# Kernel tuning notes

Hardware: AMD Instinct MI355X
Metric: run time of the kernel (lower is better)

The kernel has to match this reference:

```python
import jax, jax.numpy as jnp
import numpy as np

N = 100_000
E = 1_600_000
F_IN = 128
HID = 64
HEADS = 2
HC = HID // HEADS  # 32 per-head channels
EPS = 1e-5
NEG_SLOPE = 0.2


def _layer_norm(x, g, b):
    mu = jnp.mean(x, axis=-1, keepdims=True)
    var = jnp.mean(jnp.square(x - mu), axis=-1, keepdims=True)
    return (x - mu) * jax.lax.rsqrt(var + EPS) * g + b


def _batch_norm(x, g, b):
    # training-mode batch statistics over the node axis (biased variance)
    mu = jnp.mean(x, axis=0, keepdims=True)
    var = jnp.mean(jnp.square(x - mu), axis=0, keepdims=True)
    return (x - mu) * jax.lax.rsqrt(var + EPS) * g + b


def _gcn_conv(x, src, dst, W, bias, n):
    # PyG GCNConv: self-loops already included in (src, dst); symmetric norm
    deg = jax.ops.segment_sum(jnp.ones_like(src, dtype=x.dtype), dst, num_segments=n)
    dinv = jnp.where(deg > 0, jax.lax.rsqrt(deg), 0.0)
    norm = dinv[src] * dinv[dst]                      # [E2]
    xw = x @ W                                        # [N, out]
    msg = xw[src] * norm[:, None]                     # gather + scale
    out = jax.ops.segment_sum(msg, dst, num_segments=n)
    return out + bias


def _gat_conv(x, src, dst, W, att_src, att_dst, bias, n):
    # PyG GATConv, heads=HEADS, concat=True (self-loops included in src/dst)
    xw = (x @ W).reshape(n, HEADS, HC)                # [N, H, C]
    a_s = jnp.sum(xw * att_src, axis=-1)              # [N, H]
    a_d = jnp.sum(xw * att_dst, axis=-1)              # [N, H]
    e = jax.nn.leaky_relu(a_s[src] + a_d[dst], NEG_SLOPE)  # [E2, H]
    m = jax.ops.segment_max(e, dst, num_segments=n)   # per-target max for stability
    e = jnp.exp(e - m[dst])
    denom = jax.ops.segment_sum(e, dst, num_segments=n)
    alpha = e / (denom[dst] + 1e-16)                  # neighborhood softmax
    out = jax.ops.segment_sum(xw[src] * alpha[:, :, None], dst, num_segments=n)
    return out.reshape(n, HEADS * HC) + bias


def setup_inputs() -> dict:
    key = jax.random.key(0)
    ks = jax.random.split(key, 20)
    f32 = jnp.float32
    d = {}
    d["accessibility_features"] = jax.random.normal(ks[0], (N, F_IN), dtype=f32)
    d["edge_index"] = jax.random.randint(ks[1], (2, E), 0, N, dtype=jnp.int64)
    # LayerNorm
    d["ln_g"] = jnp.ones((F_IN,), f32); d["ln_b"] = jnp.zeros((F_IN,), f32)
    # feature encoder
    d["enc_w1"] = jax.random.normal(ks[2], (F_IN, HID), f32) * (2.0 / (F_IN + HID)) ** 0.5
    d["enc_b1"] = jnp.zeros((HID,), f32)
    d["enc_w2"] = jax.random.normal(ks[3], (HID, HID), f32) * (1.0 / HID) ** 0.5
    d["enc_b2"] = jnp.zeros((HID,), f32)
    # GCN 1
    d["gcn1_w"] = jax.random.normal(ks[4], (HID, HID), f32) * (1.0 / HID) ** 0.5
    d["gcn1_b"] = jnp.zeros((HID,), f32)
    d["bn1_g"] = jnp.ones((HID,), f32); d["bn1_b"] = jnp.zeros((HID,), f32)
    # GAT
    d["gat_w"] = jax.random.normal(ks[5], (HID, HEADS * HC), f32) * (1.0 / HID) ** 0.5
    d["gat_as"] = jax.random.normal(ks[6], (HEADS, HC), f32) * 0.1
    d["gat_ad"] = jax.random.normal(ks[7], (HEADS, HC), f32) * 0.1
    d["gat_b"] = jnp.zeros((HEADS * HC,), f32)
    d["bn2_g"] = jnp.ones((HID,), f32); d["bn2_b"] = jnp.zeros((HID,), f32)
    # GCN 2 -> hidden//2
    d["gcn2_w"] = jax.random.normal(ks[8], (HID, HID // 2), f32) * (2.0 / (HID + HID // 2)) ** 0.5
    d["gcn2_b"] = jnp.zeros((HID // 2,), f32)
    d["bn3_g"] = jnp.ones((HID // 2,), f32); d["bn3_b"] = jnp.zeros((HID // 2,), f32)
    # prediction head
    d["pred_w1"] = jax.random.normal(ks[9], (HID // 2, HID // 4), f32) * (2.0 / (HID // 2 + HID // 4)) ** 0.5
    d["pred_b1"] = jnp.zeros((HID // 4,), f32)
    d["pred_w2"] = jax.random.normal(ks[10], (HID // 4, 1), f32) * (2.0 / (HID // 4 + 1)) ** 0.5
    d["pred_b2"] = jnp.zeros((1,), f32)
    return d


def reference(accessibility_features, edge_index, ln_g, ln_b, enc_w1, enc_b1,
              enc_w2, enc_b2, gcn1_w, gcn1_b, bn1_g, bn1_b, gat_w, gat_as,
              gat_ad, gat_b, bn2_g, bn2_b, gcn2_w, gcn2_b, bn3_g, bn3_b,
              pred_w1, pred_b1, pred_w2, pred_b2):
    n = accessibility_features.shape[0]
    loops = jnp.arange(n, dtype=edge_index.dtype)
    src = jnp.concatenate([edge_index[0], loops])   # add self-loops once
    dst = jnp.concatenate([edge_index[1], loops])

    x = _layer_norm(accessibility_features, ln_g, ln_b)
    x = jax.nn.relu(x @ enc_w1 + enc_b1)            # dropout = identity (eval)
    x = jax.nn.relu(x @ enc_w2 + enc_b2)

    x = _gcn_conv(x, src, dst, gcn1_w, gcn1_b, n)
    x = jax.nn.relu(_batch_norm(x, bn1_g, bn1_b))

    xa = _gat_conv(x, src, dst, gat_w, gat_as, gat_ad, gat_b, n)
    xa = jax.nn.relu(_batch_norm(xa, bn2_g, bn2_b))

    x = _gcn_conv(xa, src, dst, gcn2_w, gcn2_b, n)
    x = jax.nn.relu(_batch_norm(x, bn3_g, bn3_b))

    h = jax.nn.relu(x @ pred_w1 + pred_b1)
    svi = jax.nn.sigmoid((h @ pred_w2 + pred_b2).squeeze(-1))
    return svi
```

## Files before the change

kernel.cpp:

```cpp
#include <hip/hip_runtime.h>
#include <math.h>

#define F_IN 128
#define HID  64
#define EPS  1e-5f
#define NSLOPE 0.2f
#define BSH 9
#define MAXBUK 1024
#define EPB 4096
#define SPB 4096

__device__ __forceinline__ float lrelu(float x) { return x > 0.f ? x : NSLOPE * x; }


__global__ __launch_bounds__(256) void k_buk_count(const int* __restrict__ ei,
                                                   int* __restrict__ bukcnt, int E, int nbuk) {
  __shared__ int lc[MAXBUK];
  for (int k = threadIdx.x; k < nbuk; k += 256) lc[k] = 0;
  __syncthreads();
  int base = blockIdx.x * EPB, end = min(E, base + EPB);
  for (int t = base + threadIdx.x; t < end; t += 256) atomicAdd(&lc[ei[E + t] >> BSH], 1);
  __syncthreads();
  for (int k = threadIdx.x; k < nbuk; k += 256)
    if (lc[k]) atomicAdd(&bukcnt[k], lc[k]);
}

__global__ void k_buk_scan(const int* __restrict__ bukcnt, int* __restrict__ bukbase, int nbuk) {
  __shared__ int l[MAXBUK + 1];
  for (int k = threadIdx.x; k < nbuk; k += blockDim.x) l[k] = bukcnt[k];
  __syncthreads();
  if (threadIdx.x == 0) {
    int r = 0;
    for (int k = 0; k < nbuk; ++k) { int t = l[k]; l[k] = r; r += t; }
    l[nbuk] = r;
  }
  __syncthreads();
  for (int k = threadIdx.x; k <= nbuk; k += blockDim.x) bukbase[k] = l[k];
}

__global__ __launch_bounds__(256) void k_buk_scatter(const int* __restrict__ ei,
                                                     const int* __restrict__ bukbase,
                                                     int* __restrict__ bukcur,
                                                     int2* __restrict__ pairs, int E, int nbuk) {
  __shared__ int lc[MAXBUK];
  __shared__ int lbase[MAXBUK];
  for (int k = threadIdx.x; k < nbuk; k += 256) lc[k] = 0;
  __syncthreads();
  int base = blockIdx.x * EPB, end = min(E, base + EPB);
  for (int t = base + threadIdx.x; t < end; t += 256) atomicAdd(&lc[ei[E + t] >> BSH], 1);
  __syncthreads();
  for (int k = threadIdx.x; k < nbuk; k += 256) {
    int c = lc[k];
    lbase[k] = c ? atomicAdd(&bukcur[k], c) : 0;
  }
  __syncthreads();
  for (int k = threadIdx.x; k < nbuk; k += 256) lc[k] = 0;
  __syncthreads();
  for (int t = base + threadIdx.x; t < end; t += 256) {
    int s = ei[t], d = ei[E + t];
    int b = d >> BSH;
    int o = atomicAdd(&lc[b], 1);
    pairs[bukbase[b] + lbase[b] + o] = make_int2(s, d);
  }
}

__global__ __launch_bounds__(256) void k_buk_deg(const int2* __restrict__ pairs,
                                                 const int* __restrict__ bukbase,
                                                 int* __restrict__ ideg, int N) {
  __shared__ int ldeg[1 << BSH];
  int b = blockIdx.x;
  for (int k = threadIdx.x; k < (1 << BSH); k += 256) ldeg[k] = 0;
  __syncthreads();
  int s0 = bukbase[b], s1 = bukbase[b + 1], nb = b << BSH;
  for (int t = s0 + threadIdx.x; t < s1; t += 256) atomicAdd(&ldeg[pairs[t].y - nb], 1);
  __syncthreads();
  for (int k = threadIdx.x; k < (1 << BSH); k += 256) {
    int node = nb + k;
    if (node < N) ideg[node] = ldeg[k];
  }
}

__global__ __launch_bounds__(256) void k_scan_sums(const int* __restrict__ ideg,
                                                   int* __restrict__ bsum, int N) {
  __shared__ int red[256];
  int base = blockIdx.x * SPB + threadIdx.x * 16;
  int s = 0;
#pragma unroll
  for (int j = 0; j < 16; ++j) { int i = base + j; if (i < N) s += ideg[i] + 1; }
  red[threadIdx.x] = s;
  __syncthreads();
  for (int o = 128; o; o >>= 1) {
    if (threadIdx.x < o) red[threadIdx.x] += red[threadIdx.x + o];
    __syncthreads();
  }
  if (threadIdx.x == 0) bsum[blockIdx.x] = red[0];
}

__global__ void k_scan_tops(int* __restrict__ bsum, int nb) {
  __shared__ int l[MAXBUK];
  for (int k = threadIdx.x; k < nb; k += blockDim.x) l[k] = bsum[k];
  __syncthreads();
  if (threadIdx.x == 0) {
    int r = 0;
    for (int k = 0; k < nb; ++k) { int t = l[k]; l[k] = r; r += t; }
  }
  __syncthreads();
  for (int k = threadIdx.x; k < nb; k += blockDim.x) bsum[k] = l[k];
}

__global__ __launch_bounds__(256) void k_scan_apply(const int* __restrict__ ideg,
                                                    const int* __restrict__ bsum,
                                                    int* __restrict__ rowstart,
                                                    float* __restrict__ dinv,
                                                    int* __restrict__ csr, int N) {
  __shared__ int pre[256];
  int base = blockIdx.x * SPB + threadIdx.x * 16;
  int deg[16];
  int s = 0;
#pragma unroll
  for (int j = 0; j < 16; ++j) {
    int i = base + j;
    int d = (i < N) ? ideg[i] + 1 : 0;
    deg[j] = d; s += d;
  }
  pre[threadIdx.x] = s;
  __syncthreads();
  for (int o = 1; o < 256; o <<= 1) {
    int v = (threadIdx.x >= o) ? pre[threadIdx.x - o] : 0;
    __syncthreads();
    pre[threadIdx.x] += v;
    __syncthreads();
  }
  int off = bsum[blockIdx.x] + pre[threadIdx.x] - s;
#pragma unroll
  for (int j = 0; j < 16; ++j) {
    int i = base + j;
    if (i < N) {
      rowstart[i] = off;
      dinv[i] = rsqrtf((float)deg[j]);
      csr[off] = i;
      off += deg[j];
    }
  }
}

__global__ __launch_bounds__(256) void k_buk_fill(const int2* __restrict__ pairs,
                                                  const int* __restrict__ bukbase,
                                                  const int* __restrict__ rowstart,
                                                  int* __restrict__ csr) {
  __shared__ int lcur[1 << BSH];
  int b = blockIdx.x;
  for (int k = threadIdx.x; k < (1 << BSH); k += 256) lcur[k] = 0;
  __syncthreads();
  int s0 = bukbase[b], s1 = bukbase[b + 1], nb = b << BSH;
  for (int t = s0 + threadIdx.x; t < s1; t += 256) {
    int2 pr = pairs[t];
    int o = atomicAdd(&lcur[pr.y - nb], 1);
    csr[rowstart[pr.y] + 1 + o] = pr.x;
  }
}

__global__ void k_precomp(const float* __restrict__ w1, const float* __restrict__ ln_g,
                          const float* __restrict__ ln_b, const float* __restrict__ b1,
                          float* __restrict__ w1g, float* __restrict__ c1,
                          float* __restrict__ cb) {
  int j = threadIdx.x;
  float c1v = 0.f, cbv = 0.f;
  for (int k = 0; k < F_IN; ++k) {
    float w = w1[k * HID + j];
    float wg = ln_g[k] * w;
    w1g[k * HID + j] = wg;
    c1v += wg;
    cbv += ln_b[k] * w;
  }
  c1[j] = c1v;
  cb[j] = cbv + b1[j];
}

__global__ __launch_bounds__(256) void k_enc(
    const float* __restrict__ x, const float* __restrict__ w1g,
    const float* __restrict__ c1, const float* __restrict__ cb,
    const float* __restrict__ w2, const float* __restrict__ b2,
    float* __restrict__ out, int N) {
  __shared__ float shl[256 * 65];
  int i = blockIdx.x * 256 + threadIdx.x;
  if (i >= N) return;
  const float4* xr = (const float4*)(x + (size_t)i * F_IN);
  float acc[HID];
#pragma unroll
  for (int j = 0; j < HID; ++j) acc[j] = 0.f;
  float s = 0.f, q = 0.f;
#pragma unroll 1
  for (int c = 0; c < F_IN / 4; ++c) {
    float4 xv = xr[c];
    s += xv.x + xv.y + xv.z + xv.w;
    q += xv.x * xv.x + xv.y * xv.y + xv.z * xv.z + xv.w * xv.w;
    const float* wr = w1g + c * 4 * HID;
#pragma unroll
    for (int e = 0; e < 4; ++e) {
      float xe = (e == 0) ? xv.x : (e == 1) ? xv.y : (e == 2) ? xv.z : xv.w;
      const float4* w4 = (const float4*)(wr + e * HID);
#pragma unroll
      for (int j4 = 0; j4 < HID / 4; ++j4) {
        float4 wv = w4[j4];
        acc[j4 * 4 + 0] += xe * wv.x;
        acc[j4 * 4 + 1] += xe * wv.y;
        acc[j4 * 4 + 2] += xe * wv.z;
        acc[j4 * 4 + 3] += xe * wv.w;
      }
    }
  }
  float mu = s * (1.f / F_IN);
  float var = q * (1.f / F_IN) - mu * mu;
  float rs = rsqrtf(var + EPS);
  int base = threadIdx.x * 65;
#pragma unroll
  for (int j = 0; j < HID; ++j)
    shl[base + j] = fmaxf(rs * (acc[j] - mu * c1[j]) + cb[j], 0.f);
  float acc2[HID];
#pragma unroll
  for (int j = 0; j < HID; ++j) acc2[j] = b2[j];
#pragma unroll 4
  for (int j = 0; j < HID; ++j) {
    float hj = shl[base + j];
    const float4* w4 = (const float4*)(w2 + j * HID);
#pragma unroll
    for (int c4 = 0; c4 < HID / 4; ++c4) {
      float4 wv = w4[c4];
      acc2[c4 * 4 + 0] += hj * wv.x;
      acc2[c4 * 4 + 1] += hj * wv.y;
      acc2[c4 * 4 + 2] += hj * wv.z;
      acc2[c4 * 4 + 3] += hj * wv.w;
    }
  }
  float4* o4 = (float4*)(out + (size_t)i * HID);
#pragma unroll
  for (int c4 = 0; c4 < HID / 4; ++c4)
    o4[c4] = make_float4(fmaxf(acc2[c4 * 4 + 0], 0.f), fmaxf(acc2[c4 * 4 + 1], 0.f),
                         fmaxf(acc2[c4 * 4 + 2], 0.f), fmaxf(acc2[c4 * 4 + 3], 0.f));
}

template <int FOUT, bool GAT, bool BNIN>
__global__ __launch_bounds__(256) void k_gemm_reg(
    const float* __restrict__ x, const float* __restrict__ w,
    const float* __restrict__ stats,
    const float* __restrict__ atts, const float* __restrict__ atd,
    float* __restrict__ out, float* __restrict__ a_s, float* __restrict__ a_d, int N) {
  int i = blockIdx.x * 256 + threadIdx.x;
  if (i >= N) return;
  const float4* xr = (const float4*)(x + (size_t)i * HID);
  float acc[FOUT];
#pragma unroll
  for (int j = 0; j < FOUT; ++j) acc[j] = 0.f;
#pragma unroll 1
  for (int c = 0; c < HID / 4; ++c) {
    float4 xv = xr[c];
    if (BNIN) {
      xv.x = fmaxf(xv.x * stats[c * 4 + 0] + stats[HID + c * 4 + 0], 0.f);
      xv.y = fmaxf(xv.y * stats[c * 4 + 1] + stats[HID + c * 4 + 1], 0.f);
      xv.z = fmaxf(xv.z * stats[c * 4 + 2] + stats[HID + c * 4 + 2], 0.f);
      xv.w = fmaxf(xv.w * stats[c * 4 + 3] + stats[HID + c * 4 + 3], 0.f);
    }
    const float* wr = w + c * 4 * FOUT;
#pragma unroll
    for (int e = 0; e < 4; ++e) {
      float xe = (e == 0) ? xv.x : (e == 1) ? xv.y : (e == 2) ? xv.z : xv.w;
      const float4* w4 = (const float4*)(wr + e * FOUT);
#pragma unroll
      for (int j4 = 0; j4 < FOUT / 4; ++j4) {
        float4 wv = w4[j4];
        acc[j4 * 4 + 0] += xe * wv.x;
        acc[j4 * 4 + 1] += xe * wv.y;
        acc[j4 * 4 + 2] += xe * wv.z;
        acc[j4 * 4 + 3] += xe * wv.w;
      }
    }
  }
  float4* o4 = (float4*)(out + (size_t)i * FOUT);
#pragma unroll
  for (int c4 = 0; c4 < FOUT / 4; ++c4)
    o4[c4] = make_float4(acc[c4 * 4 + 0], acc[c4 * 4 + 1], acc[c4 * 4 + 2], acc[c4 * 4 + 3]);
  if (GAT) {
    float s0 = 0.f, s1 = 0.f, d0 = 0.f, d1 = 0.f;
#pragma unroll
    for (int c = 0; c < 32; ++c) { s0 += acc[c] * atts[c]; d0 += acc[c] * atd[c]; }
#pragma unroll
    for (int c = 32; c < 64; ++c) { s1 += acc[c] * atts[c]; d1 += acc[c] * atd[c]; }
    a_s[i * 2] = s0; a_s[i * 2 + 1] = s1;
    a_d[i * 2] = d0; a_d[i * 2 + 1] = d1;
  }
}

__global__ __launch_bounds__(256) void k_gcn_pull64(
    const int* __restrict__ csr, const int* __restrict__ rowstart, const int* __restrict__ ideg,
    const float* __restrict__ dinv, const float* __restrict__ xw,
    float* __restrict__ out, int N) {
  int wave = threadIdx.x >> 6, lane = threadIdx.x & 63;
  int i = blockIdx.x * 4 + wave;
  if (i >= N) return;
  int row = rowstart[i], dg = ideg[i] + 1;
  float did = dinv[i];
  float acc = 0.f;
  for (int base = 0; base < dg; base += 64) {
    int cnt = min(64, dg - base);
    int sid = (lane < cnt) ? csr[row + base + lane] : 0;
    int n = 0;
    for (; n + 4 <= cnt; n += 4) {
      int s0 = __shfl(sid, n), s1 = __shfl(sid, n + 1);
      int s2 = __shfl(sid, n + 2), s3 = __shfl(sid, n + 3);
      acc += dinv[s0] * did * xw[s0 * 64 + lane] + dinv[s1] * did * xw[s1 * 64 + lane] +
             dinv[s2] * did * xw[s2 * 64 + lane] + dinv[s3] * did * xw[s3 * 64 + lane];
    }
    for (; n < cnt; ++n) {
      int s0 = __shfl(sid, n);
      acc += dinv[s0] * did * xw[s0 * 64 + lane];
    }
  }
  out[i * 64 + lane] = acc;
}

__global__ __launch_bounds__(256) void k_gcn_pull32(
    const int* __restrict__ csr, const int* __restrict__ rowstart, const int* __restrict__ ideg,
    const float* __restrict__ dinv, const float* __restrict__ xw,
    float* __restrict__ out, int N) {
  int wave = threadIdx.x >> 6, lane = threadIdx.x & 63;
  int half = lane >> 5, lf = lane & 31;
  int i = (blockIdx.x * 4 + wave) * 2 + half;
  if (i >= N) return;
  int row = rowstart[i], dg = ideg[i] + 1;
  float did = dinv[i];
  float acc = 0.f;
  for (int base = 0; base < dg; base += 32) {
    int cnt = min(32, dg - base);
    int sid = (lf < cnt) ? csr[row + base + lf] : 0;
    int n = 0;
    for (; n + 2 <= cnt; n += 2) {
      int s0 = __shfl(sid, n, 32), s1 = __shfl(sid, n + 1, 32);
      acc += dinv[s0] * did * xw[s0 * 32 + lf] + dinv[s1] * did * xw[s1 * 32 + lf];
    }
    for (; n < cnt; ++n) {
      int s0 = __shfl(sid, n, 32);
      acc += dinv[s0] * did * xw[s0 * 32 + lf];
    }
  }
  out[i * 32 + lf] = acc;
}

__global__ __launch_bounds__(256) void k_gat_attn(
    const int* __restrict__ csr, const int* __restrict__ rowstart, const int* __restrict__ ideg,
    const float* __restrict__ a_s, const float* __restrict__ a_d,
    float* __restrict__ m_, float* __restrict__ rden, int N) {
  int wave = threadIdx.x >> 6, lane = threadIdx.x & 63;
  int i = blockIdx.x * 4 + wave;
  if (i >= N) return;
  int row = rowstart[i], dg = ideg[i] + 1;
  float ad0 = a_d[i * 2], ad1 = a_d[i * 2 + 1];
  if (dg <= 64) {
    float e0 = -1e30f, e1 = -1e30f;
    if (lane < dg) {
      int s = csr[row + lane];
      e0 = lrelu(a_s[s * 2] + ad0);
      e1 = lrelu(a_s[s * 2 + 1] + ad1);
    }
    float m0 = e0, m1 = e1;
#pragma unroll
    for (int o = 32; o; o >>= 1) { m0 = fmaxf(m0, __shfl_xor(m0, o)); m1 = fmaxf(m1, __shfl_xor(m1, o)); }
    float s0 = (lane < dg) ? __expf(e0 - m0) : 0.f;
    float s1 = (lane < dg) ? __expf(e1 - m1) : 0.f;
#pragma unroll
    for (int o = 32; o; o >>= 1) { s0 += __shfl_xor(s0, o); s1 += __shfl_xor(s1, o); }
    if (lane == 0) {
      m_[i * 2] = m0; m_[i * 2 + 1] = m1;
      rden[i * 2] = 1.f / (s0 + 1e-16f); rden[i * 2 + 1] = 1.f / (s1 + 1e-16f);
    }
  } else {
    float m0 = -1e30f, m1 = -1e30f;
    for (int base = 0; base < dg; base += 64)
      if (base + lane < dg) {
        int s = csr[row + base + lane];
        m0 = fmaxf(m0, lrelu(a_s[s * 2] + ad0));
        m1 = fmaxf(m1, lrelu(a_s[s * 2 + 1] + ad1));
      }
#pragma unroll
    for (int o = 32; o; o >>= 1) { m0 = fmaxf(m0, __shfl_xor(m0, o)); m1 = fmaxf(m1, __shfl_xor(m1, o)); }
    float s0 = 0.f, s1 = 0.f;
    for (int base = 0; base < dg; base += 64)
      if (base + lane < dg) {
        int s = csr[row + base + lane];
        s0 += __expf(lrelu(a_s[s * 2] + ad0) - m0);
        s1 += __expf(lrelu(a_s[s * 2 + 1] + ad1) - m1);
      }
#pragma unroll
    for (int o = 32; o; o >>= 1) { s0 += __shfl_xor(s0, o); s1 += __shfl_xor(s1, o); }
    if (lane == 0) {
      m_[i * 2] = m0; m_[i * 2 + 1] = m1;
      rden[i * 2] = 1.f / (s0 + 1e-16f); rden[i * 2 + 1] = 1.f / (s1 + 1e-16f);
    }
  }
}

__global__ __launch_bounds__(256) void k_gat_pv(
    const int* __restrict__ csr, const int* __restrict__ rowstart, const int* __restrict__ ideg,
    const float* __restrict__ a_s, const float* __restrict__ a_d,
    const float* __restrict__ m_, const float* __restrict__ rden,
    const float* __restrict__ xw, float* __restrict__ out, int N) {
  int wave = threadIdx.x >> 6, lane = threadIdx.x & 63;
  int i = blockIdx.x * 4 + wave;
  if (i >= N) return;
  int row = rowstart[i], dg = ideg[i] + 1;
  int h = lane >> 5;
  float adh = a_d[i * 2 + h], mh = m_[i * 2 + h], rh = rden[i * 2 + h];
  float acc = 0.f;
  for (int base = 0; base < dg; base += 64) {
    int cnt = min(64, dg - base);
    int sid = (lane < cnt) ? csr[row + base + lane] : 0;
    int n = 0;
    for (; n + 2 <= cnt; n += 2) {
      int s0 = __shfl(sid, n), s1 = __shfl(sid, n + 1);
      float al0 = __expf(lrelu(a_s[s0 * 2 + h] + adh) - mh) * rh;
      float al1 = __expf(lrelu(a_s[s1 * 2 + h] + adh) - mh) * rh;
      acc += al0 * xw[s0 * HID + lane] + al1 * xw[s1 * HID + lane];
    }
    for (; n < cnt; ++n) {
      int s0 = __shfl(sid, n);
      float al0 = __expf(lrelu(a_s[s0 * 2 + h] + adh) - mh) * rh;
      acc += al0 * xw[s0 * HID + lane];
    }
  }
  out[i * HID + lane] = acc;
}

template <int F>
__global__ __launch_bounds__(256) void k_bn_reduce(const float* __restrict__ x,
                                                   float* __restrict__ partials, int N) {
  __shared__ float sS[F], sQ[F];
  int tid = threadIdx.x;
  int t = blockIdx.x * 256 + tid;
  int stride = gridDim.x * 256;
  int total4 = N * F / 4;
  int f0 = (t * 4) % F;
  float s0 = 0, s1 = 0, s2 = 0, s3 = 0, q0 = 0, q1 = 0, q2 = 0, q3 = 0;
  for (int c = t; c < total4; c += stride) {
    float4 v = ((const float4*)x)[c];
    s0 += v.x; q0 += v.x * v.x;
    s1 += v.y; q1 += v.y * v.y;
    s2 += v.z; q2 += v.z * v.z;
    s3 += v.w; q3 += v.w * v.w;
  }
  if (tid < F) { sS[tid] = 0.f; sQ[tid] = 0.f; }
  __syncthreads();
  atomicAdd(&sS[f0], s0);     atomicAdd(&sQ[f0], q0);
  atomicAdd(&sS[f0 + 1], s1); atomicAdd(&sQ[f0 + 1], q1);
  atomicAdd(&sS[f0 + 2], s2); atomicAdd(&sQ[f0 + 2], q2);
  atomicAdd(&sS[f0 + 3], s3); atomicAdd(&sQ[f0 + 3], q3);
  __syncthreads();
  if (tid < F) {
    partials[blockIdx.x * 2 * F + tid]     = sS[tid];
    partials[blockIdx.x * 2 * F + F + tid] = sQ[tid];
  }
}

template <int F>
__global__ void k_bn_finalize(const float* __restrict__ partials, int nblk,
                              float* __restrict__ stats, const float* __restrict__ g,
                              const float* __restrict__ b, int N) {
  int f = threadIdx.x;
  if (f >= F) return;
  float s = 0.f, q = 0.f;
  for (int k = 0; k < nblk; ++k) {
    s += partials[k * 2 * F + f];
    q += partials[k * 2 * F + F + f];
  }
  float mu = s / (float)N;
  float var = q / (float)N - mu * mu;
  float sc = rsqrtf(var + EPS) * g[f];
  stats[f] = sc;
  stats[F + f] = b[f] - mu * sc;
}

__global__ __launch_bounds__(256) void k_pred(
    const float* __restrict__ x, const float* __restrict__ stats,
    const float* __restrict__ w1, const float* __restrict__ b1,
    const float* __restrict__ w2, const float* __restrict__ b2,
    float* __restrict__ out, int N) {
  int i = blockIdx.x * 256 + threadIdx.x;
  if (i >= N) return;
  const float4* xr = (const float4*)(x + (size_t)i * 32);
  float acc[16];
#pragma unroll
  for (int j = 0; j < 16; ++j) acc[j] = b1[j];
#pragma unroll 1
  for (int c = 0; c < 8; ++c) {
    float4 xv = xr[c];
    xv.x = fmaxf(xv.x * stats[c * 4 + 0] + stats[32 + c * 4 + 0], 0.f);
    xv.y = fmaxf(xv.y * stats[c * 4 + 1] + stats[32 + c * 4 + 1], 0.f);
    xv.z = fmaxf(xv.z * stats[c * 4 + 2] + stats[32 + c * 4 + 2], 0.f);
    xv.w = fmaxf(xv.w * stats[c * 4 + 3] + stats[32 + c * 4 + 3], 0.f);
    const float* wr = w1 + c * 4 * 16;
#pragma unroll
    for (int e = 0; e < 4; ++e) {
      float xe = (e == 0) ? xv.x : (e == 1) ? xv.y : (e == 2) ? xv.z : xv.w;
      const float4* w4 = (const float4*)(wr + e * 16);
#pragma unroll
      for (int j4 = 0; j4 < 4; ++j4) {
        float4 wv = w4[j4];
        acc[j4 * 4 + 0] += xe * wv.x;
        acc[j4 * 4 + 1] += xe * wv.y;
        acc[j4 * 4 + 2] += xe * wv.z;
        acc[j4 * 4 + 3] += xe * wv.w;
      }
    }
  }
  float z = b2[0];
#pragma unroll
  for (int j = 0; j < 16; ++j) z += fmaxf(acc[j], 0.f) * w2[j];
  out[i] = 1.f / (1.f + __expf(-z));
}

extern "C" void kernel_launch(void* const* d_in, const int* in_sizes, int n_in,
                              void* d_out, int out_size, void* d_ws, size_t ws_size,
                              hipStream_t stream) {
  const float* x_in  = (const float*)d_in[0];
  const int*   ei    = (const int*)d_in[1];
  const float* ln_g  = (const float*)d_in[2];
  const float* ln_b  = (const float*)d_in[3];
  const float* enc_w1 = (const float*)d_in[4];
  const float* enc_b1 = (const float*)d_in[5];
  const float* enc_w2 = (const float*)d_in[6];
  const float* enc_b2 = (const float*)d_in[7];
  const float* gcn1_w = (const float*)d_in[8];
  const float* bn1_g = (const float*)d_in[10];
  const float* bn1_b = (const float*)d_in[11];
  const float* gat_w  = (const float*)d_in[12];
  const float* gat_as = (const float*)d_in[13];
  const float* gat_ad = (const float*)d_in[14];
  const float* bn2_g = (const float*)d_in[16];
  const float* bn2_b = (const float*)d_in[17];
  const float* gcn2_w = (const float*)d_in[18];
  const float* bn3_g = (const float*)d_in[20];
  const float* bn3_b = (const float*)d_in[21];
  const float* pw1 = (const float*)d_in[22];
  const float* pb1 = (const float*)d_in[23];
  const float* pw2 = (const float*)d_in[24];
  const float* pb2 = (const float*)d_in[25];
  float* out = (float*)d_out;

  int N = in_sizes[0] / F_IN;
  int E = in_sizes[1] / 2;
  int nbuk = (N + (1 << BSH) - 1) >> BSH;

  const int NBLK_BN = 128;

  char* p = (char*)d_ws;
  auto alloc = [&](size_t bytes) { char* r = p; p += (bytes + 255) & ~(size_t)255; return (void*)r; };
  float* h     = (float*)alloc((size_t)N * 64 * 4);
  float* xw    = (float*)alloc((size_t)N * 64 * 4);
  float* agg   = (float*)alloc((size_t)N * 64 * 4);
  float* as_   = (float*)alloc((size_t)N * 2 * 4);
  float* ad_   = (float*)alloc((size_t)N * 2 * 4);
  float* m_    = (float*)alloc((size_t)N * 2 * 4);
  float* rden  = (float*)alloc((size_t)N * 2 * 4);
  float* dinv  = (float*)alloc((size_t)N * 4);
  float* stats = (float*)alloc(2 * 64 * 4);
  float* parts = (float*)alloc((size_t)NBLK_BN * 2 * 64 * 4);
  float* w1g   = (float*)alloc((size_t)F_IN * HID * 4);
  float* c1    = (float*)alloc(HID * 4);
  float* cb    = (float*)alloc(HID * 4);
  int* ideg    = (int*)alloc((size_t)N * 4);
  int* rowst   = (int*)alloc((size_t)N * 4);
  int* csr     = (int*)alloc((size_t)(N + E) * 4);
  int* bukcnt  = (int*)alloc((size_t)MAXBUK * 4);
  int* bukbase = (int*)alloc((size_t)(MAXBUK + 1) * 4);
  int* bukcur  = (int*)alloc((size_t)MAXBUK * 4);
  int* bsum    = (int*)alloc((size_t)MAXBUK * 4);
  int2* pairs  = (int2*)h;

  hipMemsetAsync(bukcnt, 0, (size_t)nbuk * 4, stream);
  hipMemsetAsync(bukcur, 0, (size_t)nbuk * 4, stream);

  int EB = (E + EPB - 1) / EPB;
  int SB = (N + SPB - 1) / SPB;
  int NB = (N + 255) / 256;
  int NB4 = (N + 3) / 4;
  int NB8 = (N + 7) / 8;

  k_buk_count<<<EB, 256, 0, stream>>>(ei, bukcnt, E, nbuk);
  k_buk_scan<<<1, 256, 0, stream>>>(bukcnt, bukbase, nbuk);
  k_buk_scatter<<<EB, 256, 0, stream>>>(ei, bukbase, bukcur, pairs, E, nbuk);
  k_buk_deg<<<nbuk, 256, 0, stream>>>(pairs, bukbase, ideg, N);
  k_scan_sums<<<SB, 256, 0, stream>>>(ideg, bsum, N);
  k_scan_tops<<<1, 256, 0, stream>>>(bsum, SB);
  k_scan_apply<<<SB, 256, 0, stream>>>(ideg, bsum, rowst, dinv, csr, N);
  k_buk_fill<<<nbuk, 256, 0, stream>>>(pairs, bukbase, rowst, csr);

  k_precomp<<<1, 64, 0, stream>>>(enc_w1, ln_g, ln_b, enc_b1, w1g, c1, cb);
  k_enc<<<NB, 256, 0, stream>>>(x_in, w1g, c1, cb, enc_w2, enc_b2, h, N);

  k_gemm_reg<64, false, false><<<NB, 256, 0, stream>>>(h, gcn1_w, nullptr, nullptr, nullptr,
                                                       xw, nullptr, nullptr, N);
  k_gcn_pull64<<<NB4, 256, 0, stream>>>(csr, rowst, ideg, dinv, xw, agg, N);
  k_bn_reduce<64><<<NBLK_BN, 256, 0, stream>>>(agg, parts, N);
  k_bn_finalize<64><<<1, 64, 0, stream>>>(parts, NBLK_BN, stats, bn1_g, bn1_b, N);

  k_gemm_reg<64, true, true><<<NB, 256, 0, stream>>>(agg, gat_w, stats, gat_as, gat_ad,
                                                     xw, as_, ad_, N);
  k_gat_attn<<<NB4, 256, 0, stream>>>(csr, rowst, ideg, as_, ad_, m_, rden, N);
  k_gat_pv<<<NB4, 256, 0, stream>>>(csr, rowst, ideg, as_, ad_, m_, rden, xw, h, N);
  k_bn_reduce<64><<<NBLK_BN, 256, 0, stream>>>(h, parts, N);
  k_bn_finalize<64><<<1, 64, 0, stream>>>(parts, NBLK_BN, stats, bn2_g, bn2_b, N);

  k_gemm_reg<32, false, true><<<NB, 256, 0, stream>>>(h, gcn2_w, stats, nullptr, nullptr,
                                                      xw, nullptr, nullptr, N);
  k_gcn_pull32<<<NB8, 256, 0, stream>>>(csr, rowst, ideg, dinv, xw, agg, N);
  k_bn_reduce<32><<<NBLK_BN, 256, 0, stream>>>(agg, parts, N);
  k_bn_finalize<32><<<1, 32, 0, stream>>>(parts, NBLK_BN, stats, bn3_g, bn3_b, N);

  k_pred<<<NB, 256, 0, stream>>>(agg, stats, pw1, pb1, pw2, pb2, out, N);
}
```

Before: 628.2 us.

## Fuse GAT attention softmax and aggregation into one online-softmax kernel

Merges the separate attention-normalizer kernel and the weighted aggregation kernel into a single per-node wave kernel that uses an online softmax with running max and rescaling. Each edge's exp is computed once per lane and broadcast by shuffles instead of being recomputed per head lane, and the second CSR/a_s gather pass plus the m_/rden buffers disappear. It also raises the BN reduction block count from 128 to 512. In exchange it adds extra shuffles and rescale work per 64-edge chunk, and more partials for the finalize step to read.

```diff
diff --git a/kernel.cpp b/kernel.cpp
--- a/kernel.cpp
+++ b/kernel.cpp
@@ -346,88 +346,60 @@
   out[i * 32 + lf] = acc;
 }
 
-__global__ __launch_bounds__(256) void k_gat_attn(
+__global__ __launch_bounds__(256) void k_gat_fused(
     const int* __restrict__ csr, const int* __restrict__ rowstart, const int* __restrict__ ideg,
     const float* __restrict__ a_s, const float* __restrict__ a_d,
-    float* __restrict__ m_, float* __restrict__ rden, int N) {
-  int wave = threadIdx.x >> 6, lane = threadIdx.x & 63;
-  int i = blockIdx.x * 4 + wave;
-  if (i >= N) return;
-  int row = rowstart[i], dg = ideg[i] + 1;
-  float ad0 = a_d[i * 2], ad1 = a_d[i * 2 + 1];
-  if (dg <= 64) {
-    float e0 = -1e30f, e1 = -1e30f;
-    if (lane < dg) {
-      int s = csr[row + lane];
-      e0 = lrelu(a_s[s * 2] + ad0);
-      e1 = lrelu(a_s[s * 2 + 1] + ad1);
-    }
-    float m0 = e0, m1 = e1;
-#pragma unroll
-    for (int o = 32; o; o >>= 1) { m0 = fmaxf(m0, __shfl_xor(m0, o)); m1 = fmaxf(m1, __shfl_xor(m1, o)); }
-    float s0 = (lane < dg) ? __expf(e0 - m0) : 0.f;
-    float s1 = (lane < dg) ? __expf(e1 - m1) : 0.f;
-#pragma unroll
-    for (int o = 32; o; o >>= 1) { s0 += __shfl_xor(s0, o); s1 += __shfl_xor(s1, o); }
-    if (lane == 0) {
-      m_[i * 2] = m0; m_[i * 2 + 1] = m1;
-      rden[i * 2] = 1.f / (s0 + 1e-16f); rden[i * 2 + 1] = 1.f / (s1 + 1e-16f);
-    }
-  } else {
-    float m0 = -1e30f, m1 = -1e30f;
-    for (int base = 0; base < dg; base += 64)
-      if (base + lane < dg) {
-        int s = csr[row + base + lane];
-        m0 = fmaxf(m0, lrelu(a_s[s * 2] + ad0));
-        m1 = fmaxf(m1, lrelu(a_s[s * 2 + 1] + ad1));
-      }
-#pragma unroll
-    for (int o = 32; o; o >>= 1) { m0 = fmaxf(m0, __shfl_xor(m0, o)); m1 = fmaxf(m1, __shfl_xor(m1, o)); }
-    float s0 = 0.f, s1 = 0.f;
-    for (int base = 0; base < dg; base += 64)
-      if (base + lane < dg) {
-        int s = csr[row + base + lane];
-        s0 += __expf(lrelu(a_s[s * 2] + ad0) - m0);
-        s1 += __expf(lrelu(a_s[s * 2 + 1] + ad1) - m1);
-      }
-#pragma unroll
-    for (int o = 32; o; o >>= 1) { s0 += __shfl_xor(s0, o); s1 += __shfl_xor(s1, o); }
-    if (lane == 0) {
-      m_[i * 2] = m0; m_[i * 2 + 1] = m1;
-      rden[i * 2] = 1.f / (s0 + 1e-16f); rden[i * 2 + 1] = 1.f / (s1 + 1e-16f);
-    }
-  }
-}
-
-__global__ __launch_bounds__(256) void k_gat_pv(
-    const int* __restrict__ csr, const int* __restrict__ rowstart, const int* __restrict__ ideg,
-    const float* __restrict__ a_s, const float* __restrict__ a_d,
-    const float* __restrict__ m_, const float* __restrict__ rden,
     const float* __restrict__ xw, float* __restrict__ out, int N) {
   int wave = threadIdx.x >> 6, lane = threadIdx.x & 63;
   int i = blockIdx.x * 4 + wave;
   if (i >= N) return;
   int row = rowstart[i], dg = ideg[i] + 1;
   int h = lane >> 5;
-  float adh = a_d[i * 2 + h], mh = m_[i * 2 + h], rh = rden[i * 2 + h];
-  float acc = 0.f;
+  float ad0 = a_d[i * 2], ad1 = a_d[i * 2 + 1];
+  float m0 = -1e30f, m1 = -1e30f, z0 = 0.f, z1 = 0.f, acc = 0.f;
   for (int base = 0; base < dg; base += 64) {
     int cnt = min(64, dg - base);
     int sid = (lane < cnt) ? csr[row + base + lane] : 0;
+    float e0 = -1e30f, e1 = -1e30f;
+    if (lane < cnt) {
+      e0 = lrelu(a_s[sid * 2] + ad0);
+      e1 = lrelu(a_s[sid * 2 + 1] + ad1);
+    }
+    float cm0 = e0, cm1 = e1;
+#pragma unroll
+    for (int o = 32; o; o >>= 1) {
+      cm0 = fmaxf(cm0, __shfl_xor(cm0, o));
+      cm1 = fmaxf(cm1, __shfl_xor(cm1, o));
+    }
+    float nm0 = fmaxf(m0, cm0), nm1 = fmaxf(m1, cm1);
+    float r0 = __expf(m0 - nm0), r1 = __expf(m1 - nm1);
+    z0 *= r0; z1 *= r1;
+    acc *= (h == 0) ? r0 : r1;
+    m0 = nm0; m1 = nm1;
+    float p0 = (lane < cnt) ? __expf(e0 - m0) : 0.f;
+    float p1 = (lane < cnt) ? __expf(e1 - m1) : 0.f;
+    float s0 = p0, s1 = p1;
+#pragma unroll
+    for (int o = 32; o; o >>= 1) { s0 += __shfl_xor(s0, o); s1 += __shfl_xor(s1, o); }
+    z0 += s0; z1 += s1;
     int n = 0;
     for (; n + 2 <= cnt; n += 2) {
-      int s0 = __shfl(sid, n), s1 = __shfl(sid, n + 1);
-      float al0 = __expf(lrelu(a_s[s0 * 2 + h] + adh) - mh) * rh;
-      float al1 = __expf(lrelu(a_s[s1 * 2 + h] + adh) - mh) * rh;
-      acc += al0 * xw[s0 * HID + lane] + al1 * xw[s1 * HID + lane];
+      int v0 = __shfl(sid, n), v1 = __shfl(sid, n + 1);
+      float pa0 = __shfl(p0, n), pb0 = __shfl(p1, n);
+      float pa1 = __shfl(p0, n + 1), pb1 = __shfl(p1, n + 1);
+      float al0 = (h == 0) ? pa0 : pb0;
+      float al1 = (h == 0) ? pa1 : pb1;
+      acc += al0 * xw[v0 * HID + lane] + al1 * xw[v1 * HID + lane];
     }
     for (; n < cnt; ++n) {
-      int s0 = __shfl(sid, n);
-      float al0 = __expf(lrelu(a_s[s0 * 2 + h] + adh) - mh) * rh;
-      acc += al0 * xw[s0 * HID + lane];
-    }
-  }
-  out[i * HID + lane] = acc;
+      int v0 = __shfl(sid, n);
+      float pa0 = __shfl(p0, n), pb0 = __shfl(p1, n);
+      float al0 = (h == 0) ? pa0 : pb0;
+      acc += al0 * xw[v0 * HID + lane];
+    }
+  }
+  float zh = (h == 0) ? z0 : z1;
+  out[i * HID + lane] = acc / (zh + 1e-16f);
 }
 
 template <int F>
@@ -549,7 +521,7 @@
   int E = in_sizes[1] / 2;
   int nbuk = (N + (1 << BSH) - 1) >> BSH;
 
-  const int NBLK_BN = 128;
+  const int NBLK_BN = 512;
 
   char* p = (char*)d_ws;
   auto alloc = [&](size_t bytes) { char* r = p; p += (bytes + 255) & ~(size_t)255; return (void*)r; };
@@ -558,8 +530,6 @@
   float* agg   = (float*)alloc((size_t)N * 64 * 4);
   float* as_   = (float*)alloc((size_t)N * 2 * 4);
   float* ad_   = (float*)alloc((size_t)N * 2 * 4);
-  float* m_    = (float*)alloc((size_t)N * 2 * 4);
-  float* rden  = (float*)alloc((size_t)N * 2 * 4);
   float* dinv  = (float*)alloc((size_t)N * 4);
   float* stats = (float*)alloc(2 * 64 * 4);
   float* parts = (float*)alloc((size_t)NBLK_BN * 2 * 64 * 4);
@@ -604,8 +574,7 @@
 
   k_gemm_reg<64, true, true><<<NB, 256, 0, stream>>>(agg, gat_w, stats, gat_as, gat_ad,
                                                      xw, as_, ad_, N);
-  k_gat_attn<<<NB4, 256, 0, stream>>>(csr, rowst, ideg, as_, ad_, m_, rden, N);
-  k_gat_pv<<<NB4, 256, 0, stream>>>(csr, rowst, ideg, as_, ad_, m_, rden, xw, h, N);
+  k_gat_fused<<<NB4, 256, 0, stream>>>(csr, rowst, ideg, as_, ad_, xw, h, N);
   k_bn_reduce<64><<<NBLK_BN, 256, 0, stream>>>(h, parts, N);
   k_bn_finalize<64><<<1, 64, 0, stream>>>(parts, NBLK_BN, stats, bn2_g, bn2_b, N);
 
```

After: 876.0 us. 39.5% more time.
